# Optimization experiments

Measured on AMD Instinct MI355X. Metric: run time of the kernel, lower is better.

Reference implementation:

```python
import jax, jax.numpy as jnp
import numpy as np

UNITS = 256
EPS = 0.01
GAMMA = 0.01
BETA = 0.8
ALPHA = 1.0


def setup_inputs() -> dict:
    key = jax.random.key(0)
    k1, k2, k3, k4 = jax.random.split(key, 4)
    x = jax.random.normal(k1, (64, 2048, 256), dtype=jnp.float32)
    C = jax.random.normal(k2, (UNITS, UNITS), dtype=jnp.float32) * 0.05
    B = jax.random.normal(k3, (UNITS, UNITS), dtype=jnp.float32) * 0.05
    U = jax.random.normal(k4, (256, UNITS), dtype=jnp.float32) * 0.05
    b = jnp.zeros((UNITS,), dtype=jnp.float32)
    return {"x": x, "C": C, "B": B, "U": U, "b": b}


def reference(x, C, B, U, b):
    # Loop-invariant matrices (skew/symmetric mix minus gamma*I), built once.
    I = jnp.eye(UNITS, dtype=x.dtype)
    A = BETA * (B - B.T) + (1.0 - BETA) * (B + B.T) - GAMMA * I
    W = BETA * (C - C.T) + (1.0 - BETA) * (C + C.T) - GAMMA * I

    # Precompute input projection for all timesteps: [batch, T, units]
    xu = jnp.einsum('bti,iu->btu', x, U) + b
    xu_t = jnp.swapaxes(xu, 0, 1)  # [T, batch, units] for scan

    h0 = jnp.zeros((x.shape[0], UNITS), dtype=x.dtype)

    def step(h, xu_step):
        h_new = h + EPS * ALPHA * (h @ A) + EPS * jnp.tanh(h @ W + xu_step)
        return h_new, h_new

    _, hs = jax.lax.scan(step, h0, xu_t)  # hs: [T, batch, units]
    return jnp.swapaxes(hs, 0, 1)  # [batch, T, units]
```

## Files before the change

### kernel.cpp

```cpp
#include <hip/hip_runtime.h>

#define EPS 0.01f
#define TSTEPS 2048
#define BATCH 64
#define TWOLOG2E 2.8853900817779268f

typedef _Float16 half8 __attribute__((ext_vector_type(8)));
typedef _Float16 half4 __attribute__((ext_vector_type(4)));
typedef float f32x4 __attribute__((ext_vector_type(4)));

#define LDS_BARRIER() asm volatile("s_waitcnt lgkmcnt(0)\n\ts_barrier" ::: "memory")

__global__ void prep_mc_pack(const float* __restrict__ Bm, const float* __restrict__ Cm,
                             _Float16* __restrict__ mcPack) {
    int f = blockIdx.x;
    int lane = threadIdx.x;
    int w = f >> 5;
    int mt = (f >> 3) & 3;
    int kk = f & 7;
    const float* Src = (mt < 2) ? Bm : Cm;
    float scale = (mt < 2) ? 1.0f : TWOLOG2E;
    int c = 32 * w + 16 * (mt & 1) + (lane & 15);
    int k0 = kk * 32 + (lane >> 4) * 8;
    long off = ((long)f * 64 + lane) * 8;
#pragma unroll
    for (int j = 0; j < 8; ++j) {
        int k = k0 + j;
        float diag = (k == c) ? 0.01f : 0.0f;
        float v = scale * (Src[(long)k * 256 + c] - 0.6f * Src[(long)c * 256 + k] - diag);
        mcPack[off + j] = (_Float16)v;
    }
}

__global__ void pack_u(const float* __restrict__ U, _Float16* __restrict__ up) {
    int t = blockIdx.x * 64 + threadIdx.x;
    int lane = t & 63;
    int tile = t >> 6;
    int nn = tile & 15;
    int kk = tile >> 4;
    int krow = kk * 32 + (lane >> 4) * 8;
    int col = nn * 16 + (lane & 15);
    long off = (long)t * 8;
#pragma unroll
    for (int jj = 0; jj < 8; ++jj) {
        up[off + jj] = (_Float16)U[(krow + jj) * 256 + col];
    }
}

__global__ __launch_bounds__(256) void xu_gemm(const float* __restrict__ x,
                                               const _Float16* __restrict__ up,
                                               const float* __restrict__ bias,
                                               float* __restrict__ out) {
    int wave = threadIdx.x >> 6;
    int lane = threadIdx.x & 63;
    int m = lane & 15;
    int quad = lane >> 4;
    long row0 = (long)blockIdx.x * 64 + wave * 16;
    const float* xrow = x + (row0 + m) * 256 + quad * 8;

    f32x4 acc[16];
#pragma unroll
    for (int nn = 0; nn < 16; ++nn) acc[nn] = (f32x4){0.f, 0.f, 0.f, 0.f};

#pragma unroll
    for (int kk = 0; kk < 8; ++kk) {
        f32x4 xa = *(const f32x4*)(xrow + kk * 32);
        f32x4 xb = *(const f32x4*)(xrow + kk * 32 + 4);
        half8 af;
        af[0] = (_Float16)xa[0]; af[1] = (_Float16)xa[1];
        af[2] = (_Float16)xa[2]; af[3] = (_Float16)xa[3];
        af[4] = (_Float16)xb[0]; af[5] = (_Float16)xb[1];
        af[6] = (_Float16)xb[2]; af[7] = (_Float16)xb[3];
        const _Float16* ub = up + ((long)kk * 1024 + lane) * 8;
#pragma unroll
        for (int nn = 0; nn < 16; ++nn) {
            half8 bf = *(const half8*)(ub + (long)nn * 512);
            acc[nn] = __builtin_amdgcn_mfma_f32_16x16x32_f16(af, bf, acc[nn], 0, 0, 0);
        }
    }
#pragma unroll
    for (int nn = 0; nn < 16; ++nn) {
        int col = nn * 16 + m;
        float bv = bias[col];
#pragma unroll
        for (int i = 0; i < 4; ++i) {
            out[(row0 + quad * 4 + i) * 256 + col] = (acc[nn][i] + bv) * TWOLOG2E;
        }
    }
}

__global__ __launch_bounds__(512, 2) void scan_kernel(const _Float16* __restrict__ mcPack,
                                                      float* __restrict__ io) {
    const int tid = threadIdx.x;
    const int w = tid >> 6;
    const int lane = tid & 63;
    const int m = lane & 15;
    const int q = lane >> 4;
    const int b0 = blockIdx.x * 16;

    half8 mcf[4][8];
#pragma unroll
    for (int mt = 0; mt < 4; ++mt)
#pragma unroll
        for (int kk = 0; kk < 8; ++kk)
            mcf[mt][kk] = *(const half8*)(mcPack + (((long)(w * 4 + mt) * 8 + kk) * 64 + lane) * 8);

    __shared__ _Float16 hB[2][4096];

    {
        half8 z = (half8)(_Float16)0.0f;
        *(half8*)(&hB[0][tid * 8]) = z;
    }

    const int rdIdx = lane * 8;
    const int wrIdx = 512 * w + 8 * m + 128 * (q >> 1) + 4 * (q & 1);

    float* p = io + ((long)(b0 + m) * TSTEPS) * 256 + 32 * w + 4 * q;

    f32x4 hs[2];
    hs[0] = (f32x4){0.f, 0.f, 0.f, 0.f};
    hs[1] = (f32x4){0.f, 0.f, 0.f, 0.f};

    f32x4 xq[2][2];
#pragma unroll
    for (int mt = 0; mt < 2; ++mt) {
        xq[0][mt] = *(const f32x4*)(p + mt * 16);
        xq[1][mt] = *(const f32x4*)(p + 256 + mt * 16);
    }
    __syncthreads();

    auto step = [&](int t, const _Float16* hbR, _Float16* hbW, f32x4 (&xc)[2]) {
        half8 hb[8];
#pragma unroll
        for (int kk = 0; kk < 8; ++kk)
            hb[kk] = *(const half8*)(hbR + kk * 512 + rdIdx);

        f32x4 aA = __builtin_amdgcn_mfma_f32_16x16x32_f16(mcf[0][0], hb[0], hs[0], 0, 0, 0);
        f32x4 aW = __builtin_amdgcn_mfma_f32_16x16x32_f16(mcf[2][0], hb[0], xc[0], 0, 0, 0);
#pragma unroll
        for (int kk = 1; kk < 8; ++kk) {
            aA = __builtin_amdgcn_mfma_f32_16x16x32_f16(mcf[0][kk], hb[kk], aA, 0, 0, 0);
            aW = __builtin_amdgcn_mfma_f32_16x16x32_f16(mcf[2][kk], hb[kk], aW, 0, 0, 0);
        }
        f32x4 bA = __builtin_amdgcn_mfma_f32_16x16x32_f16(mcf[1][0], hb[0], hs[1], 0, 0, 0);
        f32x4 bW = __builtin_amdgcn_mfma_f32_16x16x32_f16(mcf[3][0], hb[0], xc[1], 0, 0, 0);
#pragma unroll
        for (int kk = 1; kk < 8; ++kk) {
            bA = __builtin_amdgcn_mfma_f32_16x16x32_f16(mcf[1][kk], hb[kk], bA, 0, 0, 0);
            bW = __builtin_amdgcn_mfma_f32_16x16x32_f16(mcf[3][kk], hb[kk], bW, 0, 0, 0);
        }

        {
            f32x4 hn;
#pragma unroll
            for (int i = 0; i < 4; ++i) {
                float e = __builtin_amdgcn_exp2f(aW[i]);
                float r = __builtin_amdgcn_rcpf(e + 1.0f);
                float hsv = fmaf(-2.0f, r, aA[i] + 1.0f);
                hs[0][i] = hsv;
                hn[i] = EPS * hsv;
            }
            half4 h4;
#pragma unroll
            for (int i = 0; i < 4; ++i) h4[i] = (_Float16)hn[i];
            *(half4*)(hbW + wrIdx) = h4;
            *(f32x4*)(p) = hn;
        }
        {
            f32x4 hn;
#pragma unroll
            for (int i = 0; i < 4; ++i) {
                float e = __builtin_amdgcn_exp2f(bW[i]);
                float r = __builtin_amdgcn_rcpf(e + 1.0f);
                float hsv = fmaf(-2.0f, r, bA[i] + 1.0f);
                hs[1][i] = hsv;
                hn[i] = EPS * hsv;
            }
            half4 h4;
#pragma unroll
            for (int i = 0; i < 4; ++i) h4[i] = (_Float16)hn[i];
            *(half4*)(hbW + wrIdx + 256) = h4;
            *(f32x4*)(p + 16) = hn;
        }

        if (t + 2 < TSTEPS) {
#pragma unroll
            for (int mt = 0; mt < 2; ++mt)
                xc[mt] = *(const f32x4*)(p + 512 + mt * 16);
        }
        p += 256;
        LDS_BARRIER();
    };

    for (int t = 0; t < TSTEPS; t += 2) {
        step(t, hB[0], hB[1], xq[0]);
        step(t + 1, hB[1], hB[0], xq[1]);
    }
}

extern "C" void kernel_launch(void* const* d_in, const int* in_sizes, int n_in,
                              void* d_out, int out_size, void* d_ws, size_t ws_size,
                              hipStream_t stream) {
    const float* x    = (const float*)d_in[0];
    const float* C    = (const float*)d_in[1];
    const float* Bm   = (const float*)d_in[2];
    const float* U    = (const float*)d_in[3];
    const float* bias = (const float*)d_in[4];
    float* out = (float*)d_out;

    _Float16* mcPack = (_Float16*)d_ws;
    _Float16* up     = (_Float16*)((char*)d_ws + 262144);

    prep_mc_pack<<<256, 64, 0, stream>>>(Bm, C, mcPack);
    pack_u<<<128, 64, 0, stream>>>(U, up);
    xu_gemm<<<2048, 256, 0, stream>>>(x, up, bias, out);
    scan_kernel<<<4, 512, 0, stream>>>(mcPack, out);
}
```

Before: 2.219 ms.

## Split scan work across 16 waves, one 16-column tile per wave

The recurrent scan kernel now runs 1024 threads (16 waves) per block instead of 512, so each wave computes one 16-unit output tile rather than two. This halves the MFMA chain per wave per step and the register-resident weight fragments, which shortens the serial critical path of each timestep. The weight packing kernel and the LDS write indexing are remapped to match. In exchange, a 16-wave barrier runs every step, and the LDS reads of h are duplicated across twice as many waves.

```diff
diff --git a/kernel.cpp b/kernel.cpp
--- a/kernel.cpp
+++ b/kernel.cpp
@@ -15,12 +15,12 @@
                              _Float16* __restrict__ mcPack) {
     int f = blockIdx.x;
     int lane = threadIdx.x;
-    int w = f >> 5;
-    int mt = (f >> 3) & 3;
+    int w = f >> 4;
+    int mt = (f >> 3) & 1;
     int kk = f & 7;
-    const float* Src = (mt < 2) ? Bm : Cm;
-    float scale = (mt < 2) ? 1.0f : TWOLOG2E;
-    int c = 32 * w + 16 * (mt & 1) + (lane & 15);
+    const float* Src = (mt == 0) ? Bm : Cm;
+    float scale = (mt == 0) ? 1.0f : TWOLOG2E;
+    int c = 16 * w + (lane & 15);
     int k0 = kk * 32 + (lane >> 4) * 8;
     long off = ((long)f * 64 + lane) * 8;
 #pragma unroll
@@ -89,8 +89,8 @@
     }
 }
 
-__global__ __launch_bounds__(512, 2) void scan_kernel(const _Float16* __restrict__ mcPack,
-                                                      float* __restrict__ io) {
+__global__ __launch_bounds__(1024, 4) void scan_kernel(const _Float16* __restrict__ mcPack,
+                                                       float* __restrict__ io) {
     const int tid = threadIdx.x;
     const int w = tid >> 6;
     const int lane = tid & 63;
@@ -98,95 +98,78 @@
     const int q = lane >> 4;
     const int b0 = blockIdx.x * 16;
 
-    half8 mcf[4][8];
-#pragma unroll
-    for (int mt = 0; mt < 4; ++mt)
+    half8 mcf[2][8];
+#pragma unroll
+    for (int mt = 0; mt < 2; ++mt)
 #pragma unroll
         for (int kk = 0; kk < 8; ++kk)
-            mcf[mt][kk] = *(const half8*)(mcPack + (((long)(w * 4 + mt) * 8 + kk) * 64 + lane) * 8);
+            mcf[mt][kk] = *(const half8*)(mcPack + (((long)(w * 2 + mt) * 8 + kk) * 64 + lane) * 8);
 
     __shared__ _Float16 hB[2][4096];
 
     {
-        half8 z = (half8)(_Float16)0.0f;
-        *(half8*)(&hB[0][tid * 8]) = z;
+        half4 z = (half4)(_Float16)0.0f;
+        *(half4*)(&hB[0][tid * 4]) = z;
     }
 
     const int rdIdx = lane * 8;
-    const int wrIdx = 512 * w + 8 * m + 128 * (q >> 1) + 4 * (q & 1);
-
-    float* p = io + ((long)(b0 + m) * TSTEPS) * 256 + 32 * w + 4 * q;
-
-    f32x4 hs[2];
-    hs[0] = (f32x4){0.f, 0.f, 0.f, 0.f};
-    hs[1] = (f32x4){0.f, 0.f, 0.f, 0.f};
-
-    f32x4 xq[2][2];
-#pragma unroll
-    for (int mt = 0; mt < 2; ++mt) {
-        xq[0][mt] = *(const f32x4*)(p + mt * 16);
-        xq[1][mt] = *(const f32x4*)(p + 256 + mt * 16);
-    }
+    const int wrIdx = 512 * (w >> 1) + 256 * (w & 1) + 128 * (q >> 1) + 8 * m + 4 * (q & 1);
+
+    float* p = io + ((long)(b0 + m) * TSTEPS) * 256 + 16 * w + 4 * q;
+
+    f32x4 hs = (f32x4){0.f, 0.f, 0.f, 0.f};
+
+    f32x4 xq[2];
+    xq[0] = *(const f32x4*)(p);
+    xq[1] = *(const f32x4*)(p + 256);
     __syncthreads();
 
-    auto step = [&](int t, const _Float16* hbR, _Float16* hbW, f32x4 (&xc)[2]) {
-        half8 hb[8];
-#pragma unroll
-        for (int kk = 0; kk < 8; ++kk)
-            hb[kk] = *(const half8*)(hbR + kk * 512 + rdIdx);
-
-        f32x4 aA = __builtin_amdgcn_mfma_f32_16x16x32_f16(mcf[0][0], hb[0], hs[0], 0, 0, 0);
-        f32x4 aW = __builtin_amdgcn_mfma_f32_16x16x32_f16(mcf[2][0], hb[0], xc[0], 0, 0, 0);
-#pragma unroll
-        for (int kk = 1; kk < 8; ++kk) {
-            aA = __builtin_amdgcn_mfma_f32_16x16x32_f16(mcf[0][kk], hb[kk], aA, 0, 0, 0);
-            aW = __builtin_amdgcn_mfma_f32_16x16x32_f16(mcf[2][kk], hb[kk], aW, 0, 0, 0);
-        }
-        f32x4 bA = __builtin_amdgcn_mfma_f32_16x16x32_f16(mcf[1][0], hb[0], hs[1], 0, 0, 0);
-        f32x4 bW = __builtin_amdgcn_mfma_f32_16x16x32_f16(mcf[3][0], hb[0], xc[1], 0, 0, 0);
-#pragma unroll
-        for (int kk = 1; kk < 8; ++kk) {
-            bA = __builtin_amdgcn_mfma_f32_16x16x32_f16(mcf[1][kk], hb[kk], bA, 0, 0, 0);
-            bW = __builtin_amdgcn_mfma_f32_16x16x32_f16(mcf[3][kk], hb[kk], bW, 0, 0, 0);
-        }
-
-        {
-            f32x4 hn;
-#pragma unroll
-            for (int i = 0; i < 4; ++i) {
-                float e = __builtin_amdgcn_exp2f(aW[i]);
-                float r = __builtin_amdgcn_rcpf(e + 1.0f);
-                float hsv = fmaf(-2.0f, r, aA[i] + 1.0f);
-                hs[0][i] = hsv;
-                hn[i] = EPS * hsv;
-            }
-            half4 h4;
-#pragma unroll
-            for (int i = 0; i < 4; ++i) h4[i] = (_Float16)hn[i];
-            *(half4*)(hbW + wrIdx) = h4;
-            *(f32x4*)(p) = hn;
-        }
-        {
-            f32x4 hn;
-#pragma unroll
-            for (int i = 0; i < 4; ++i) {
-                float e = __builtin_amdgcn_exp2f(bW[i]);
-                float r = __builtin_amdgcn_rcpf(e + 1.0f);
-                float hsv = fmaf(-2.0f, r, bA[i] + 1.0f);
-                hs[1][i] = hsv;
-                hn[i] = EPS * hsv;
-            }
-            half4 h4;
-#pragma unroll
-            for (int i = 0; i < 4; ++i) h4[i] = (_Float16)hn[i];
-            *(half4*)(hbW + wrIdx + 256) = h4;
-            *(f32x4*)(p + 16) = hn;
-        }
+    auto step = [&](int t, const _Float16* hbR, _Float16* hbW, f32x4& xc) {
+        half8 hb0 = *(const half8*)(hbR + 0 * 512 + rdIdx);
+        half8 hb1 = *(const half8*)(hbR + 1 * 512 + rdIdx);
+        half8 hb2 = *(const half8*)(hbR + 2 * 512 + rdIdx);
+        half8 hb3 = *(const half8*)(hbR + 3 * 512 + rdIdx);
+
+        f32x4 aA = __builtin_amdgcn_mfma_f32_16x16x32_f16(mcf[0][0], hb0, hs, 0, 0, 0);
+        f32x4 aW = __builtin_amdgcn_mfma_f32_16x16x32_f16(mcf[1][0], hb0, xc, 0, 0, 0);
+        aA = __builtin_amdgcn_mfma_f32_16x16x32_f16(mcf[0][1], hb1, aA, 0, 0, 0);
+        aW = __builtin_amdgcn_mfma_f32_16x16x32_f16(mcf[1][1], hb1, aW, 0, 0, 0);
+        aA = __builtin_amdgcn_mfma_f32_16x16x32_f16(mcf[0][2], hb2, aA, 0, 0, 0);
+        aW = __builtin_amdgcn_mfma_f32_16x16x32_f16(mcf[1][2], hb2, aW, 0, 0, 0);
+        aA = __builtin_amdgcn_mfma_f32_16x16x32_f16(mcf[0][3], hb3, aA, 0, 0, 0);
+        aW = __builtin_amdgcn_mfma_f32_16x16x32_f16(mcf[1][3], hb3, aW, 0, 0, 0);
+
+        half8 hb4 = *(const half8*)(hbR + 4 * 512 + rdIdx);
+        half8 hb5 = *(const half8*)(hbR + 5 * 512 + rdIdx);
+        half8 hb6 = *(const half8*)(hbR + 6 * 512 + rdIdx);
+        half8 hb7 = *(const half8*)(hbR + 7 * 512 + rdIdx);
+
+        aA = __builtin_amdgcn_mfma_f32_16x16x32_f16(mcf[0][4], hb4, aA, 0, 0, 0);
+        aW = __builtin_amdgcn_mfma_f32_16x16x32_f16(mcf[1][4], hb4, aW, 0, 0, 0);
+        aA = __builtin_amdgcn_mfma_f32_16x16x32_f16(mcf[0][5], hb5, aA, 0, 0, 0);
+        aW = __builtin_amdgcn_mfma_f32_16x16x32_f16(mcf[1][5], hb5, aW, 0, 0, 0);
+        aA = __builtin_amdgcn_mfma_f32_16x16x32_f16(mcf[0][6], hb6, aA, 0, 0, 0);
+        aW = __builtin_amdgcn_mfma_f32_16x16x32_f16(mcf[1][6], hb6, aW, 0, 0, 0);
+        aA = __builtin_amdgcn_mfma_f32_16x16x32_f16(mcf[0][7], hb7, aA, 0, 0, 0);
+        aW = __builtin_amdgcn_mfma_f32_16x16x32_f16(mcf[1][7], hb7, aW, 0, 0, 0);
+
+        f32x4 hn;
+#pragma unroll
+        for (int i = 0; i < 4; ++i) {
+            float e = __builtin_amdgcn_exp2f(aW[i]);
+            float r = __builtin_amdgcn_rcpf(e + 1.0f);
+            float hsv = fmaf(-2.0f, r, aA[i] + 1.0f);
+            hs[i] = hsv;
+            hn[i] = EPS * hsv;
+        }
+        half4 h4;
+#pragma unroll
+        for (int i = 0; i < 4; ++i) h4[i] = (_Float16)hn[i];
+        *(half4*)(hbW + wrIdx) = h4;
+        *(f32x4*)(p) = hn;
 
         if (t + 2 < TSTEPS) {
-#pragma unroll
-            for (int mt = 0; mt < 2; ++mt)
-                xc[mt] = *(const f32x4*)(p + 512 + mt * 16);
+            xc = *(const f32x4*)(p + 512);
         }
         p += 256;
         LDS_BARRIER();
@@ -214,5 +197,5 @@
     prep_mc_pack<<<256, 64, 0, stream>>>(Bm, C, mcPack);
     pack_u<<<128, 64, 0, stream>>>(U, up);
     xu_gemm<<<2048, 256, 0, stream>>>(x, up, bias, out);
-    scan_kernel<<<4, 512, 0, stream>>>(mcPack, out);
-}
+    scan_kernel<<<4, 1024, 0, stream>>>(mcPack, out);
+}
```

After: 2.233 ms. No clear change (+0.6%).
